# Performance work log

Hardware: AMD Instinct MI355X
Metric: run time of the kernel (lower is better)

## Reference

```python
import jax, jax.numpy as jnp
import numpy as np

GAMMA = 1.05  # VoxelSampler.GAMMA


def setup_inputs() -> dict:
    key = jax.random.key(0)
    k1, k2, k3, k4, k5 = jax.random.split(key, 5)
    B, T, R, Np, F = 2, 8, 128, 32768, 5
    # point xy within pc_range, remaining features (z, intensity, ...) gaussian
    xy = jax.random.uniform(k1, (B, T, Np, 2), minval=-75.0, maxval=75.0)
    rest = jax.random.normal(k2, (B, T, Np, F - 2))
    points = jnp.concatenate([xy, rest], axis=-1)  # [B,T,Np,5]
    # rois: [cx,cy,cz, dx,dy,dz, yaw, vx,vy]
    ctr = jax.random.uniform(k3, (B, T, R, 3), minval=-75.0, maxval=75.0)
    dims = jax.random.uniform(k4, (B, T, R, 3), minval=1.0, maxval=6.0)
    yaw_vel = jax.random.normal(k5, (B, T, R, 3))
    trajectory_rois = jnp.concatenate([ctr, dims, yaw_vel], axis=-1)  # [B,T,R,9]
    return {"points": points, "trajectory_rois": trajectory_rois, "num_sample": 32}


def reference(points, trajectory_rois, num_sample):
    # points: [B,T,Np,5] (pre-partitioned per batch/frame, mirrors the
    # batch-column + timestamp masking of the torch code with static shapes)
    # trajectory_rois: [B,T,R,9]
    B, T, R, _ = trajectory_rois.shape
    Fdim = points.shape[-1]
    # speed = ||roi[..., -2:]||, per-roi gamma = clamp((1.05*(1+speed))**(t/5), max=2.5)
    speed = jnp.linalg.norm(trajectory_rois[..., 7:9], axis=-1)          # [B,T,R]
    t_idx = jnp.arange(T, dtype=points.dtype)
    gamma = jnp.minimum((GAMMA * (1.0 + speed)) ** (t_idx[None, :, None] / 5.0), 2.5)
    # cylindrical radius per roi: ||dims_xy/2|| * gamma
    radiis = jnp.linalg.norm(trajectory_rois[..., 3:5] * 0.5, axis=-1) * gamma  # [B,T,R]
    cx = trajectory_rois[..., 0]
    cy = trajectory_rois[..., 1]
    px = points[..., 0]
    py = points[..., 1]
    dx = px[:, :, None, :] - cx[..., None]   # [B,T,R,Np]
    dy = py[:, :, None, :] - cy[..., None]
    dis = jnp.sqrt(dx * dx + dy * dy)        # [B,T,R,Np]
    in_radius = (dis <= radiis[..., None]).astype(points.dtype)
    # topk over 0/1 mask: picks num_sample in-radius points (lowest indices first),
    # exactly like torch.topk(point_mask.float(), num_sample)
    vals, idx = jax.lax.top_k(in_radius, num_sample)  # [B,T,R,S]
    sampled = jnp.take_along_axis(points[:, :, None, :, :], idx[..., None], axis=3)  # [B,T,R,S,5]
    sampled = jnp.where(vals[..., None] > 0, sampled, jnp.zeros((), dtype=points.dtype))
    # stack frames -> permute(0,2,1,3,4) -> flatten(2,3): [B,R,T*S,5]
    out = jnp.transpose(sampled, (0, 2, 1, 3, 4)).reshape(B, R, T * num_sample, Fdim)
    return out
```

## Files before the change

kernel.cpp:

```cpp
#include <hip/hip_runtime.h>
#include <math.h>

#define B_   2
#define T_   8
#define R_   128
#define NP_  32768
#define F_   5
#define S_   32
#define NBT  (B_ * T_)
#define NROW (NBT * R_)
#define WV_  8
#define RPB  4
#define NBLK (NROW / RPB)
#define SEGPTS (NP_ / WV_)
#define NIT  (SEGPTS / 512)

__device__ __forceinline__ int mbcnt64(unsigned long long m) {
    return __builtin_amdgcn_mbcnt_hi((unsigned)(m >> 32),
           __builtin_amdgcn_mbcnt_lo((unsigned)m, 0u));
}

__global__ __launch_bounds__(256) void xy_transpose_prep(
    const float* __restrict__ points,
    const float* __restrict__ rois,
    float2* __restrict__ xy,
    float4* __restrict__ rowc)
{
    const int j = blockIdx.x * blockDim.x + threadIdx.x;
    if (j < NBT * NP_ / 4) {
        const float4* src = (const float4*)points + (size_t)j * 5;
        const float4 a = src[0], b = src[1], c = src[2], d = src[3], e = src[4];
        float4* dst = (float4*)xy + (size_t)j * 2;
        dst[0] = make_float4(a.x, a.y, b.y, b.z);
        dst[1] = make_float4(c.z, c.w, d.w, e.x);
    }
    if (j < NROW) {
        const int row = j;
        const int bt  = row / R_;
        const int t   = bt % T_;
        const float* roi = rois + (size_t)row * 9;
        const float cx = roi[0], cy = roi[1];
        const float hx = roi[3] * 0.5f, hy = roi[4] * 0.5f;
        const float vx = roi[7], vy = roi[8];
        const float speed  = sqrtf(vx * vx + vy * vy);
        const float base_g = 1.05f * (1.0f + speed);
        const float expo   = (float)t / 5.0f;
        const float gamma  = fminf((float)pow((double)base_g, (double)expo), 2.5f);
        const float radius = sqrtf(hx * hx + hy * hy) * gamma;
        unsigned ut = __float_as_uint(radius * radius);
        while (sqrtf(__uint_as_float(ut)) > radius) --ut;
        while (sqrtf(__uint_as_float(ut + 1u)) <= radius) ++ut;
        rowc[row] = make_float4(cx, cy, __uint_as_float(ut), 0.0f);
    }
}


#define PROC1(qq, base, rc, sel, hb)                                              \
    {                                                                             \
        const float ax = __fsub_rn(qq.x, rc.x), ay = __fsub_rn(qq.y, rc.y);       \
        const float bx = __fsub_rn(qq.z, rc.x), by = __fsub_rn(qq.w, rc.y);       \
        const float d2a = __fadd_rn(__fmul_rn(ax, ax), __fmul_rn(ay, ay));        \
        const float d2b = __fadd_rn(__fmul_rn(bx, bx), __fmul_rn(by, by));        \
        const bool p0 = (d2a <= rc.z), p1 = (d2b <= rc.z);                        \
        const unsigned long long m0 = __ballot(p0), m1 = __ballot(p1);            \
        if (m0 | m1) {                                                            \
            const int bb = sel + mbcnt64(m0) + mbcnt64(m1);                       \
            if (p0 && bb < S_) hb[bb] = (unsigned short)((base) + l2);            \
            if (p1) { const int s2 = bb + (p0 ? 1 : 0);                           \
                      if (s2 < S_) hb[s2] = (unsigned short)((base) + l2 + 1); }  \
            sel += __popcll(m0) + __popcll(m1);                                   \
        }                                                                         \
    }

#define PROCQ(qq, kk, ib)                                                         \
    PROC1(qq, (ib) + (kk) * 128, rc0, sel0, hb0)                                  \
    PROC1(qq, (ib) + (kk) * 128, rc1, sel1, hb1)                                  \
    PROC1(qq, (ib) + (kk) * 128, rc2, sel2, hb2)                                  \
    PROC1(qq, (ib) + (kk) * 128, rc3, sel3, hb3)

#define LOAD4(r0, r1, r2, r3)                                                     \
    r0 = src[0]; r1 = src[64]; r2 = src[128]; r3 = src[192]; src += 256;

#define ITER(r0, r1, r2, r3, ib)                                                  \
    PROCQ(r0, 0, ib) PROCQ(r1, 1, ib) PROCQ(r2, 2, ib) PROCQ(r3, 3, ib)

__global__ __launch_bounds__(512, 4) void fused_scan_emit(
    const float2* __restrict__ xy,
    const float4* __restrict__ rowc,
    const float* __restrict__ points,
    float* __restrict__ out)
{
    __shared__ unsigned short hitbuf[WV_][RPB][S_];
    __shared__ int cnt[WV_][RPB];
    const int w    = threadIdx.x >> 6;
    const int lane = threadIdx.x & 63;
    const int l2   = lane * 2;
    const int row0 = blockIdx.x * RPB;
    const int bt   = row0 / R_;
    const float4 rc0 = rowc[row0], rc1 = rowc[row0 + 1];
    const float4 rc2 = rowc[row0 + 2], rc3 = rowc[row0 + 3];
    unsigned short* hb0 = hitbuf[w][0];
    unsigned short* hb1 = hitbuf[w][1];
    unsigned short* hb2 = hitbuf[w][2];
    unsigned short* hb3 = hitbuf[w][3];
    const int segbase = w * SEGPTS;

    const float4* src = (const float4*)(xy + (size_t)bt * NP_) + (segbase >> 1) + lane;
    int sel0 = 0, sel1 = 0, sel2 = 0, sel3 = 0;

    float4 a0, a1, a2, a3, b0, b1, b2, b3;
    LOAD4(a0, a1, a2, a3)
    int ib = segbase;
    #pragma unroll 1
    for (int it = 0; it < NIT - 2; it += 2) {
        LOAD4(b0, b1, b2, b3)
        ITER(a0, a1, a2, a3, ib)
        LOAD4(a0, a1, a2, a3)
        ITER(b0, b1, b2, b3, ib + 512)
        ib += 1024;
    }
    LOAD4(b0, b1, b2, b3)
    ITER(a0, a1, a2, a3, ib)
    ITER(b0, b1, b2, b3, ib + 512)

    if (lane == 0) {
        cnt[w][0] = (sel0 < S_) ? sel0 : S_;
        cnt[w][1] = (sel1 < S_) ? sel1 : S_;
        cnt[w][2] = (sel2 < S_) ? sel2 : S_;
        cnt[w][3] = (sel3 < S_) ? sel3 : S_;
    }
    __syncthreads();

    if (threadIdx.x < RPB * S_) {
        const int ri = threadIdx.x >> 5;
        const int s  = threadIdx.x & 31;
        int seg = -1, local = 0, acc = 0;
        #pragma unroll
        for (int g = 0; g < WV_; ++g) {
            const int na = acc + cnt[g][ri];
            if (seg < 0 && s < na) { seg = g; local = s - acc; }
            acc = na;
        }
        const int row = row0 + ri;
        const int r = row % R_;
        const int t = bt % T_;
        const int b = bt / T_;
        float* o = out + ((((size_t)b * R_ + r) * T_ + t) * S_ + s) * (size_t)F_;
        if (seg >= 0) {
            const int pi = hitbuf[seg][ri][local];
            const float* p = points + ((size_t)bt * NP_ + pi) * F_;
            o[0] = p[0]; o[1] = p[1]; o[2] = p[2]; o[3] = p[3]; o[4] = p[4];
        } else {
            o[0] = 0.0f; o[1] = 0.0f; o[2] = 0.0f; o[3] = 0.0f; o[4] = 0.0f;
        }
    }
}

extern "C" void kernel_launch(void* const* d_in, const int* in_sizes, int n_in,
                              void* d_out, int out_size, void* d_ws, size_t ws_size,
                              hipStream_t stream) {
    const float* points = (const float*)d_in[0];
    const float* rois   = (const float*)d_in[1];
    float* out = (float*)d_out;

    char* ws = (char*)d_ws;
    float2* xy   = (float2*)ws;
    float4* rowc = (float4*)(ws + 4194304);

    xy_transpose_prep<<<(NBT * NP_ / 4 + 255) / 256, 256, 0, stream>>>(points, rois, xy, rowc);

    fused_scan_emit<<<NBLK, 512, 0, stream>>>(xy, rowc, points, out);
}
```

Measured before the change: 84.81 us.

## Pack xy as SoA pairs for packed-FP32 math and halve rows per block

The prep kernel now writes each pair of points as (x0,x1,y0,y1) so the scan can compute distances with 2-wide float vectors that may map to packed FP32 instructions. Contraction is disabled to keep the distance rounding bit-exact with the reference. Each block now handles 2 ROI rows instead of 4, doubling the block count and raising the occupancy hint to 8. The trade-off is that the xy stream is read twice as often, while each block carries less register state and the grid has more parallelism.

```diff
diff --git a/kernel.cpp b/kernel.cpp
--- a/kernel.cpp
+++ b/kernel.cpp
@@ -10,10 +10,10 @@
 #define NBT  (B_ * T_)
 #define NROW (NBT * R_)
 #define WV_  8
-#define RPB  4
-#define NBLK (NROW / RPB)
 #define SEGPTS (NP_ / WV_)
 #define NIT  (SEGPTS / 512)
+
+typedef float f2 __attribute__((ext_vector_type(2)));
 
 __device__ __forceinline__ int mbcnt64(unsigned long long m) {
     return __builtin_amdgcn_mbcnt_hi((unsigned)(m >> 32),
@@ -23,16 +23,16 @@
 __global__ __launch_bounds__(256) void xy_transpose_prep(
     const float* __restrict__ points,
     const float* __restrict__ rois,
-    float2* __restrict__ xy,
+    float4* __restrict__ xy,
     float4* __restrict__ rowc)
 {
     const int j = blockIdx.x * blockDim.x + threadIdx.x;
     if (j < NBT * NP_ / 4) {
         const float4* src = (const float4*)points + (size_t)j * 5;
         const float4 a = src[0], b = src[1], c = src[2], d = src[3], e = src[4];
-        float4* dst = (float4*)xy + (size_t)j * 2;
-        dst[0] = make_float4(a.x, a.y, b.y, b.z);
-        dst[1] = make_float4(c.z, c.w, d.w, e.x);
+        float4* dst = xy + (size_t)j * 2;
+        dst[0] = make_float4(a.x, b.y, a.y, b.z);
+        dst[1] = make_float4(c.z, d.w, c.w, e.x);
     }
     if (j < NROW) {
         const int row = j;
@@ -57,11 +57,11 @@
 
 #define PROC1(qq, base, rc, sel, hb)                                              \
     {                                                                             \
-        const float ax = __fsub_rn(qq.x, rc.x), ay = __fsub_rn(qq.y, rc.y);       \
-        const float bx = __fsub_rn(qq.z, rc.x), by = __fsub_rn(qq.w, rc.y);       \
-        const float d2a = __fadd_rn(__fmul_rn(ax, ax), __fmul_rn(ay, ay));        \
-        const float d2b = __fadd_rn(__fmul_rn(bx, bx), __fmul_rn(by, by));        \
-        const bool p0 = (d2a <= rc.z), p1 = (d2b <= rc.z);                        \
+        const f2 px = {qq.x, qq.y}, py = {qq.z, qq.w};                            \
+        const f2 dx = px - (f2){rc.x, rc.x};                                      \
+        const f2 dy = py - (f2){rc.y, rc.y};                                      \
+        const f2 d2 = dx * dx + dy * dy;          \
+        const bool p0 = (d2.x <= rc.z), p1 = (d2.y <= rc.z);                      \
         const unsigned long long m0 = __ballot(p0), m1 = __ballot(p1);            \
         if (m0 | m1) {                                                            \
             const int bb = sel + mbcnt64(m0) + mbcnt64(m1);                       \
@@ -74,9 +74,7 @@
 
 #define PROCQ(qq, kk, ib)                                                         \
     PROC1(qq, (ib) + (kk) * 128, rc0, sel0, hb0)                                  \
-    PROC1(qq, (ib) + (kk) * 128, rc1, sel1, hb1)                                  \
-    PROC1(qq, (ib) + (kk) * 128, rc2, sel2, hb2)                                  \
-    PROC1(qq, (ib) + (kk) * 128, rc3, sel3, hb3)
+    PROC1(qq, (ib) + (kk) * 128, rc1, sel1, hb1)
 
 #define LOAD4(r0, r1, r2, r3)                                                     \
     r0 = src[0]; r1 = src[64]; r2 = src[128]; r3 = src[192]; src += 256;
@@ -84,29 +82,28 @@
 #define ITER(r0, r1, r2, r3, ib)                                                  \
     PROCQ(r0, 0, ib) PROCQ(r1, 1, ib) PROCQ(r2, 2, ib) PROCQ(r3, 3, ib)
 
-__global__ __launch_bounds__(512, 4) void fused_scan_emit(
-    const float2* __restrict__ xy,
+__global__ __launch_bounds__(512, 8) void fused_scan_emit(
+    const float4* __restrict__ xy,
     const float4* __restrict__ rowc,
     const float* __restrict__ points,
     float* __restrict__ out)
 {
-    __shared__ unsigned short hitbuf[WV_][RPB][S_];
-    __shared__ int cnt[WV_][RPB];
+#pragma clang fp contract(off)
+    __shared__ unsigned short hitbuf[WV_][2][S_];
+    __shared__ int cnt[WV_][2];
     const int w    = threadIdx.x >> 6;
     const int lane = threadIdx.x & 63;
     const int l2   = lane * 2;
-    const int row0 = blockIdx.x * RPB;
+    const int row0 = blockIdx.x * 2;
+    const int row1 = row0 + 1;
     const int bt   = row0 / R_;
-    const float4 rc0 = rowc[row0], rc1 = rowc[row0 + 1];
-    const float4 rc2 = rowc[row0 + 2], rc3 = rowc[row0 + 3];
+    const float4 rc0 = rowc[row0], rc1 = rowc[row1];
     unsigned short* hb0 = hitbuf[w][0];
     unsigned short* hb1 = hitbuf[w][1];
-    unsigned short* hb2 = hitbuf[w][2];
-    unsigned short* hb3 = hitbuf[w][3];
     const int segbase = w * SEGPTS;
 
-    const float4* src = (const float4*)(xy + (size_t)bt * NP_) + (segbase >> 1) + lane;
-    int sel0 = 0, sel1 = 0, sel2 = 0, sel3 = 0;
+    const float4* src = xy + ((size_t)bt * NP_ + segbase) / 2 + lane;
+    int sel0 = 0, sel1 = 0;
 
     float4 a0, a1, a2, a3, b0, b1, b2, b3;
     LOAD4(a0, a1, a2, a3)
@@ -126,28 +123,26 @@
     if (lane == 0) {
         cnt[w][0] = (sel0 < S_) ? sel0 : S_;
         cnt[w][1] = (sel1 < S_) ? sel1 : S_;
-        cnt[w][2] = (sel2 < S_) ? sel2 : S_;
-        cnt[w][3] = (sel3 < S_) ? sel3 : S_;
     }
     __syncthreads();
 
-    if (threadIdx.x < RPB * S_) {
-        const int ri = threadIdx.x >> 5;
-        const int s  = threadIdx.x & 31;
+    if (threadIdx.x < 64) {
+        const int half = lane >> 5;
+        const int s    = lane & 31;
         int seg = -1, local = 0, acc = 0;
         #pragma unroll
         for (int g = 0; g < WV_; ++g) {
-            const int na = acc + cnt[g][ri];
+            const int na = acc + cnt[g][half];
             if (seg < 0 && s < na) { seg = g; local = s - acc; }
             acc = na;
         }
-        const int row = row0 + ri;
+        const int row = half ? row1 : row0;
         const int r = row % R_;
         const int t = bt % T_;
         const int b = bt / T_;
         float* o = out + ((((size_t)b * R_ + r) * T_ + t) * S_ + s) * (size_t)F_;
         if (seg >= 0) {
-            const int pi = hitbuf[seg][ri][local];
+            const int pi = hitbuf[seg][half][local];
             const float* p = points + ((size_t)bt * NP_ + pi) * F_;
             o[0] = p[0]; o[1] = p[1]; o[2] = p[2]; o[3] = p[3]; o[4] = p[4];
         } else {
@@ -164,10 +159,10 @@
     float* out = (float*)d_out;
 
     char* ws = (char*)d_ws;
-    float2* xy   = (float2*)ws;
+    float4* xy   = (float4*)ws;
     float4* rowc = (float4*)(ws + 4194304);
 
     xy_transpose_prep<<<(NBT * NP_ / 4 + 255) / 256, 256, 0, stream>>>(points, rois, xy, rowc);
 
-    fused_scan_emit<<<NBLK, 512, 0, stream>>>(xy, rowc, points, out);
+    fused_scan_emit<<<NROW / 2, 512, 0, stream>>>(xy, rowc, points, out);
 }
```

Measured after the change: 83.19 us. About the same (-1.9%).
